# Optimization experiments

Hardware: AMD Instinct MI355X
Metric: run time of the kernel (lower is better)

## Reference

```python
import jax, jax.numpy as jnp
import numpy as np

B, S, D, H = 2, 2048, 2048, 16
HD = D // H  # 128, head_dim (even, as asserted)
MAX_POS = 2048


def setup_inputs() -> dict:
    key = jax.random.key(0)
    ks = jax.random.split(key, 5)
    x = jax.random.normal(ks[0], (B, S, D), jnp.float32)
    Wq = jax.random.normal(ks[1], (D, D), jnp.float32) * 0.02
    Wk = jax.random.normal(ks[2], (D, D), jnp.float32) * 0.02
    Wv = jax.random.normal(ks[3], (D, D), jnp.float32) * 0.02
    Wo = jax.random.normal(ks[4], (D, D), jnp.float32) * 0.02
    # standard RoPE tables: [MAX_POS, HD]
    inv_freq = 1.0 / (10000.0 ** (jnp.arange(0, HD, 2, dtype=jnp.float32) / HD))
    angles = jnp.arange(MAX_POS, dtype=jnp.float32)[:, None] * inv_freq  # [P, HD/2]
    emb = jnp.concatenate([angles, angles], axis=-1)  # [P, HD]
    cos_freqs = jnp.cos(emb)
    sin_freqs = jnp.sin(emb)
    position_ids = jnp.broadcast_to(jnp.arange(S, dtype=jnp.int32), (B, S))
    return {"x": x, "cos_freqs": cos_freqs, "sin_freqs": sin_freqs,
            "Wq": Wq, "Wk": Wk, "Wv": Wv, "Wo": Wo,
            "position_ids": position_ids}


def _apply_rope(t, cos, sin, position_ids):
    # t: [b, s, h, hd]; cos/sin: [P, hd]; position_ids: [b, s]
    c = cos[position_ids][:, :, None, :]  # [b, s, 1, hd]
    s_ = sin[position_ids][:, :, None, :]
    t1, t2 = jnp.split(t, 2, axis=-1)
    rot = jnp.concatenate([-t2, t1], axis=-1)  # rotate-half
    return t * c + rot * s_


def reference(x, cos_freqs, sin_freqs, Wq, Wk, Wv, Wo, position_ids):
    b, s, d = x.shape
    q = (x @ Wq).reshape(b, s, H, HD)
    k = (x @ Wk).reshape(b, s, H, HD)  # n_kv_heads == n_heads
    v = (x @ Wv).reshape(b, s, H, HD)
    q = _apply_rope(q, cos_freqs, sin_freqs, position_ids)
    k = _apply_rope(k, cos_freqs, sin_freqs, position_ids)
    # [b, h, s, hd]
    q_t = jnp.swapaxes(q, 1, 2)
    k_t = jnp.swapaxes(k, 1, 2)
    v_t = jnp.swapaxes(v, 1, 2)
    scale = 1.0 / jnp.sqrt(jnp.float32(HD))
    scores = jnp.einsum('bhsd,bhtd->bhst', q_t, k_t) * scale  # O(s^2) matrix
    causal = jnp.tril(jnp.ones((s, s), dtype=bool))
    scores = jnp.where(causal[None, None, :, :], scores, -1e9)
    weights = jax.nn.softmax(scores, axis=-1)
    out = jnp.einsum('bhst,bhtd->bhsd', weights, v_t)
    out = jnp.swapaxes(out, 1, 2).reshape(b, s, d)
    out = out @ Wo
    return (out, k, v)  # kv_cache is post-RoPE, pre-transpose as in original
```

## Files before the change

kernel.cpp:

```cpp
#include <hip/hip_runtime.h>
#include <hip/hip_bf16.h>
#include <math.h>

#define B_ 2
#define S_ 2048
#define D_ 2048
#define H_ 16
#define HD_ 128
#define M_ (B_*S_)
#define BSD ((size_t)B_*S_*D_)

typedef short bf16x8 __attribute__((ext_vector_type(8)));
typedef float floatx4 __attribute__((ext_vector_type(4)));
typedef __hip_bfloat16 bf16;

union cv8 { bf16 h[8]; uint4 u; bf16x8 v; };

__device__ inline cv8 cvt8(const float4 a, const float4 b) {
    cv8 c;
    c.h[0] = __float2bfloat16(a.x); c.h[1] = __float2bfloat16(a.y);
    c.h[2] = __float2bfloat16(a.z); c.h[3] = __float2bfloat16(a.w);
    c.h[4] = __float2bfloat16(b.x); c.h[5] = __float2bfloat16(b.y);
    c.h[6] = __float2bfloat16(b.z); c.h[7] = __float2bfloat16(b.w);
    return c;
}

__device__ __forceinline__ void gld16(const void* g, void* l) {
    __builtin_amdgcn_global_load_lds(
        (const __attribute__((address_space(1))) unsigned int*)g,
        (__attribute__((address_space(3))) unsigned int*)l,
        16, 0, 0);
}

__global__ __launch_bounds__(256) void transpose_w(
    const float* __restrict__ W, bf16* __restrict__ Wt, int N, int K)
{
    __shared__ float T[32][33];
    const int k0 = blockIdx.x * 32, n0 = blockIdx.y * 32;
    const int r = threadIdx.x >> 3, c4 = (threadIdx.x & 7) * 4;
    float4 v = *(const float4*)&W[(size_t)(k0 + r) * N + n0 + c4];
    T[r][c4+0] = v.x; T[r][c4+1] = v.y; T[r][c4+2] = v.z; T[r][c4+3] = v.w;
    __syncthreads();
    union { bf16 h[4]; uint2 u; } o;
    #pragma unroll
    for (int i = 0; i < 4; ++i) o.h[i] = __float2bfloat16(T[c4 + i][r]);
    *(uint2*)&Wt[(size_t)(n0 + r) * K + k0 + c4] = o.u;
}

__global__ __launch_bounds__(256) void transpose_w_s(
    const float* __restrict__ W, bf16* __restrict__ Wt, int N, int K)
{
    __shared__ float T[32][33];
    const int k0 = blockIdx.x * 32, n0 = blockIdx.y * 32;
    const int r = threadIdx.x >> 3, c4 = (threadIdx.x & 7) * 4;
    float4 v = *(const float4*)&W[(size_t)(k0 + r) * N + n0 + c4];
    T[r][c4+0] = v.x; T[r][c4+1] = v.y; T[r][c4+2] = v.z; T[r][c4+3] = v.w;
    __syncthreads();
    union { bf16 h[4]; uint2 u; } o;
    #pragma unroll
    for (int i = 0; i < 4; ++i) o.h[i] = __float2bfloat16(T[c4 + i][r]);
    const int n = n0 + r;
    size_t bo = (size_t)n * (size_t)K * 2 + ((unsigned)((k0 + c4) * 2) ^ ((n & 3) << 4));
    *(uint2*)((char*)Wt + bo) = o.u;
}

__global__ __launch_bounds__(256) void pack_bf16(
    const float* __restrict__ src, bf16* __restrict__ dst)
{
    const size_t i = ((size_t)blockIdx.x * 256 + threadIdx.x) * 8;
    cv8 c = cvt8(*(const float4*)(src + i), *(const float4*)(src + i + 4));
    size_t bo = i * 2;
    bo ^= (size_t)(((bo >> 12) & 3) << 4);
    *(uint4*)((char*)dst + bo) = c.u;
}

__global__ __launch_bounds__(256) void rope_pack_k(
    float* __restrict__ k, bf16* __restrict__ kbb,
    const float* __restrict__ cf, const float* __restrict__ sf,
    const int* __restrict__ pos)
{
    const int idx = blockIdx.x * 256 + threadIdx.x;
    const int dg = idx & 7;
    const int h  = (idx >> 3) & (H_-1);
    const int bs = idx >> 7;
    const int s  = bs & (S_-1);
    const int b  = bs >> 11;
    const int p  = pos[bs];
    const size_t base = (size_t)bs * D_ + h*HD_ + dg*8;
    float lo[8], hi[8], c1[8], s1[8], c2[8], s2[8];
    *(float4*)&lo[0] = *(const float4*)&k[base];
    *(float4*)&lo[4] = *(const float4*)&k[base + 4];
    *(float4*)&hi[0] = *(const float4*)&k[base + 64];
    *(float4*)&hi[4] = *(const float4*)&k[base + 68];
    const float* cp = cf + (size_t)p*HD_ + dg*8;
    const float* sp = sf + (size_t)p*HD_ + dg*8;
    *(float4*)&c1[0] = *(const float4*)cp;        *(float4*)&c1[4] = *(const float4*)(cp + 4);
    *(float4*)&s1[0] = *(const float4*)sp;        *(float4*)&s1[4] = *(const float4*)(sp + 4);
    *(float4*)&c2[0] = *(const float4*)(cp + 64); *(float4*)&c2[4] = *(const float4*)(cp + 68);
    *(float4*)&s2[0] = *(const float4*)(sp + 64); *(float4*)&s2[4] = *(const float4*)(sp + 68);
    float nl[8], nh[8];
    #pragma unroll
    for (int j = 0; j < 8; ++j) {
        nl[j] = lo[j]*c1[j] - hi[j]*s1[j];
        nh[j] = hi[j]*c2[j] + lo[j]*s2[j];
    }
    *(float4*)&k[base]      = *(float4*)&nl[0];
    *(float4*)&k[base + 4]  = *(float4*)&nl[4];
    *(float4*)&k[base + 64] = *(float4*)&nh[0];
    *(float4*)&k[base + 68] = *(float4*)&nh[4];
    cv8 clo, chi;
    #pragma unroll
    for (int j = 0; j < 8; ++j) {
        clo.h[j] = __float2bfloat16(nl[j]);
        chi.h[j] = __float2bfloat16(nh[j]);
    }
    const size_t rowb = ((size_t)(b*H_ + h)*S_ + s) * (size_t)(HD_*2);
    *(uint4*)((char*)kbb + rowb + ((dg*16)       ^ ((s & 7) << 4))) = clo.u;
    *(uint4*)((char*)kbb + rowb + (((dg+8)*16)   ^ ((s & 7) << 4))) = chi.u;
}

__global__ __launch_bounds__(256) void pack_vt(
    const float* __restrict__ src, bf16* __restrict__ dst)
{
    __shared__ float T[32][33];
    const int s0 = blockIdx.x * 32;
    const int d0 = blockIdx.y * 32;
    const int bh = blockIdx.z;
    const int b = bh >> 4, h = bh & (H_-1);
    const int r = threadIdx.x >> 3, c4 = (threadIdx.x & 7) * 4;
    float4 v = *(const float4*)&src[((size_t)(b*S_ + s0 + r)*H_ + h)*HD_ + d0 + c4];
    T[r][c4+0] = v.x; T[r][c4+1] = v.y; T[r][c4+2] = v.z; T[r][c4+3] = v.w;
    __syncthreads();
    union { bf16 h4[4]; uint2 u; } o;
    #pragma unroll
    for (int i = 0; i < 4; ++i) o.h4[i] = __float2bfloat16(T[c4 + i][r]);
    const int hd = d0 + r;
    size_t rowb = ((size_t)bh*HD_ + hd) * (size_t)(S_*2);
    size_t colb = (size_t)(s0 + c4) * 2;
    colb = (colb & ~(size_t)127) | (((unsigned)colb & 127u) ^ (unsigned)((hd & 7) << 4));
    *(uint2*)((char*)dst + rowb + colb) = o.u;
}

__global__ __launch_bounds__(256, 3) void gemm_bb2(
    const bf16* __restrict__ A, const bf16* __restrict__ Wt,
    float* __restrict__ C, int M, int N, int K)
{
    __shared__ __align__(16) bf16 As[128][32];
    __shared__ __align__(16) bf16 Bs[128][32];
    const int nwg = (int)(gridDim.x * gridDim.y);
    int id = (int)(blockIdx.y * gridDim.x + blockIdx.x);
    if ((nwg & 7) == 0) id = (id & 7) * (nwg >> 3) + (id >> 3);
    const int m0 = (id % (int)gridDim.x) * 128;
    const int n0 = (id / (int)gridDim.x) * 128;
    const int tid = threadIdx.x, lane = tid & 63, w = tid >> 6;
    const int quad = lane >> 4, l16 = lane & 15;
    const int wrow = (w >> 1) * 64, wcol = (w & 1) * 64;
    const size_t K2 = (size_t)K * 2;

    floatx4 acc[4][4] = {};

    const char* Ab = (const char*)A;
    const char* Bb = (const char*)Wt;
    char* AsB = (char*)&As[0][0];
    char* BsB = (char*)&Bs[0][0];
    const int srow = lane >> 2;
    const int scol = (lane & 3) * 16;

    for (int kt = 0; kt < K; kt += 32) {
        #pragma unroll
        for (int j = 0; j < 2; ++j) {
            const int row = w*32 + j*16 + srow;
            gld16(Ab + (size_t)(m0 + row)*K2 + (size_t)(kt*2) + scol,
                  AsB + w*2048 + j*1024);
            gld16(Bb + (size_t)(n0 + row)*K2 + (size_t)(kt*2) + scol,
                  BsB + w*2048 + j*1024);
        }
        __syncthreads();

        bf16x8 af[4], bfr[4];
        #pragma unroll
        for (int t = 0; t < 4; ++t) {
            const int ra = wrow + t*16 + l16;
            af[t]  = *(const bf16x8*)(AsB + ra*64 + ((quad*16) ^ ((ra & 3) << 4)));
            const int rb = wcol + t*16 + l16;
            bfr[t] = *(const bf16x8*)(BsB + rb*64 + ((quad*16) ^ ((rb & 3) << 4)));
        }
        #pragma unroll
        for (int mt = 0; mt < 4; ++mt)
            #pragma unroll
            for (int nt = 0; nt < 4; ++nt)
                acc[mt][nt] = __builtin_amdgcn_mfma_f32_16x16x32_bf16(
                    af[mt], bfr[nt], acc[mt][nt], 0, 0, 0);
        __syncthreads();
    }

    #pragma unroll
    for (int mt = 0; mt < 4; ++mt)
        #pragma unroll
        for (int nt = 0; nt < 4; ++nt)
            #pragma unroll
            for (int r = 0; r < 4; ++r)
                C[(size_t)(m0 + wrow + mt*16 + quad*4 + r) * N
                  + n0 + wcol + nt*16 + l16] = acc[mt][nt][r];
}

__global__ __launch_bounds__(256) void gemm_xw(
    const float* __restrict__ A, const bf16* __restrict__ Wt,
    float* __restrict__ C, int M, int N, int K)
{
    __shared__ __align__(16) bf16 As[128][40];
    __shared__ __align__(16) bf16 Bs[128][40];
    const int m0 = blockIdx.x * 128, n0 = blockIdx.y * 128;
    const int tid = threadIdx.x, lane = tid & 63, w = tid >> 6;
    const int quad = lane >> 4, l16 = lane & 15;
    const int wrow = (w >> 1) * 64, wcol = (w & 1) * 64;
    floatx4 acc[4][4] = {};
    const int arow = tid >> 2;
    const int acol = (tid & 3) * 8;
    for (int kt = 0; kt < K; kt += 32) {
        #pragma unroll
        for (int p = 0; p < 2; ++p) {
            const int r = p*64 + arow;
            const float* ap = &A[(size_t)(m0 + r) * K + kt + acol];
            cv8 ca = cvt8(*(const float4*)ap, *(const float4*)(ap + 4));
            *(uint4*)&As[r][acol] = ca.u;
            const bf16* bp = &Wt[(size_t)(n0 + r) * K + kt + acol];
            *(uint4*)&Bs[r][acol] = *(const uint4*)bp;
        }
        __syncthreads();
        bf16x8 af[4], bfr[4];
        #pragma unroll
        for (int t = 0; t < 4; ++t) {
            af[t]  = *(const bf16x8*)&As[wrow + t*16 + l16][quad*8];
            bfr[t] = *(const bf16x8*)&Bs[wcol + t*16 + l16][quad*8];
        }
        #pragma unroll
        for (int mt = 0; mt < 4; ++mt)
            #pragma unroll
            for (int nt = 0; nt < 4; ++nt)
                acc[mt][nt] = __builtin_amdgcn_mfma_f32_16x16x32_bf16(
                    af[mt], bfr[nt], acc[mt][nt], 0, 0, 0);
        __syncthreads();
    }
    #pragma unroll
    for (int mt = 0; mt < 4; ++mt)
        #pragma unroll
        for (int nt = 0; nt < 4; ++nt)
            #pragma unroll
            for (int r = 0; r < 4; ++r)
                C[(size_t)(m0 + wrow + mt*16 + quad*4 + r) * N
                  + n0 + wcol + nt*16 + l16] = acc[mt][nt][r];
}

__global__ __launch_bounds__(256) void gemm_f32(
    const float* __restrict__ A, const float* __restrict__ W,
    float* __restrict__ C, int M, int N, int K)
{
    __shared__ __align__(16) bf16 As[64][40];
    __shared__ __align__(16) bf16 Bs[64][40];
    const int m0 = blockIdx.x * 64, n0 = blockIdx.y * 64;
    const int tid = threadIdx.x, lane = tid & 63, w = tid >> 6;
    const int quad = lane >> 4, l16 = lane & 15;
    const int wrow = (w >> 1) * 32, wcol = (w & 1) * 32;
    floatx4 acc[2][2] = {};
    const int ar = tid >> 2, ac = (tid & 3) * 8;
    const int br = tid >> 3, bc = (tid & 7) * 8;
    for (int kt = 0; kt < K; kt += 32) {
        {
            const float* ap = &A[(size_t)(m0 + ar) * K + kt + ac];
            cv8 c = cvt8(*(const float4*)ap, *(const float4*)(ap + 4));
            *(uint4*)&As[ar][ac] = c.u;
        }
        {
            const float* wp = &W[(size_t)(kt + br) * N + n0 + bc];
            cv8 c = cvt8(*(const float4*)wp, *(const float4*)(wp + 4));
            #pragma unroll
            for (int i = 0; i < 8; ++i) Bs[bc + i][br] = c.h[i];
        }
        __syncthreads();
        bf16x8 af[2], bfr[2];
        #pragma unroll
        for (int t = 0; t < 2; ++t) {
            af[t]  = *(const bf16x8*)&As[wrow + t*16 + l16][quad*8];
            bfr[t] = *(const bf16x8*)&Bs[wcol + t*16 + l16][quad*8];
        }
        #pragma unroll
        for (int mt = 0; mt < 2; ++mt)
            #pragma unroll
            for (int nt = 0; nt < 2; ++nt)
                acc[mt][nt] = __builtin_amdgcn_mfma_f32_16x16x32_bf16(
                    af[mt], bfr[nt], acc[mt][nt], 0, 0, 0);
        __syncthreads();
    }
    #pragma unroll
    for (int mt = 0; mt < 2; ++mt)
        #pragma unroll
        for (int nt = 0; nt < 2; ++nt)
            #pragma unroll
            for (int r = 0; r < 4; ++r)
                C[(size_t)(m0 + wrow + mt*16 + quad*4 + r) * N
                  + n0 + wcol + nt*16 + l16] = acc[mt][nt][r];
}

__global__ __launch_bounds__(256) void rope_kernel(
    float* __restrict__ q, float* __restrict__ k,
    const float* __restrict__ cf, const float* __restrict__ sf,
    const int* __restrict__ pos)
{
    const int PAIRS = B_*S_*H_*(HD_/2);
    int idx = blockIdx.x * 256 + threadIdx.x;
    float* t = q;
    if (idx >= PAIRS) { t = k; idx -= PAIRS; }
    const int d  = idx & 63;
    const int h  = (idx >> 6) & (H_-1);
    const int bs = idx >> 10;
    const int p  = pos[bs];
    const float c1 = cf[p*HD_ + d],      s1 = sf[p*HD_ + d];
    const float c2 = cf[p*HD_ + d + 64], s2 = sf[p*HD_ + d + 64];
    const size_t base = (size_t)bs * D_ + h*HD_ + d;
    const float t1 = t[base], t2 = t[base + 64];
    t[base]      = t1*c1 - t2*s1;
    t[base + 64] = t2*c2 + t1*s2;
}

__global__ __launch_bounds__(256, 2) void flash_attn_v5(
    const float* __restrict__ qg, const bf16* __restrict__ kb,
    const bf16* __restrict__ vb, bf16* __restrict__ ob,
    const float* __restrict__ cf, const float* __restrict__ sf,
    const int* __restrict__ pos)
{
    __shared__ __align__(16) bf16 Ks[2][64][128];
    __shared__ __align__(16) bf16 Vt[2][128][64];
    __shared__ __align__(16) bf16 Ps[4][16][72];

    const int qi = (int)gridDim.x - 1 - (int)blockIdx.x;
    const int q0 = qi * 64;
    const int bh = blockIdx.y;
    const int b = bh >> 4, h = bh & (H_-1);
    const int tid = threadIdx.x, lane = tid & 63, w = tid >> 6;
    const int quad = lane >> 4, l16 = lane & 15;

    const char* kbase = (const char*)(kb + (size_t)bh * S_ * HD_);
    const char* vbase = (const char*)(vb + (size_t)bh * HD_ * S_);
    char* ksd = (char*)&Ks[0][0][0];
    char* vtd = (char*)&Vt[0][0][0];

    const int klofs = w*4096;
    const int vrow0 = w*32 + (lane >> 3);
    const int vcb   = (lane & 7) * 16;

    #pragma unroll
    for (int j = 0; j < 4; ++j)
        gld16(kbase + klofs + j*1024 + lane*16, ksd + klofs + j*1024);
    #pragma unroll
    for (int j = 0; j < 4; ++j)
        gld16(vbase + (size_t)(vrow0 + j*8)*(S_*2) + vcb, vtd + w*4096 + j*1024);

    const int qrow = q0 + w*16 + l16;
    const float* qptr = qg + ((size_t)(b*S_ + qrow))*D_ + h*HD_;
    float rq[4][8];
    #pragma unroll
    for (int c = 0; c < 4; ++c) {
        const float* qp = qptr + c*32 + quad*8;
        *(float4*)&rq[c][0] = *(const float4*)qp;
        *(float4*)&rq[c][4] = *(const float4*)(qp + 4);
    }
    const int p = pos[b*S_ + qrow];
    bf16x8 qf[4];
    #pragma unroll
    for (int c = 0; c < 4; ++c) {
        const float* cp = cf + (size_t)p*HD_ + c*32 + quad*8;
        const float* sp = sf + (size_t)p*HD_ + c*32 + quad*8;
        float cc[8], ss[8];
        *(float4*)&cc[0] = *(const float4*)cp; *(float4*)&cc[4] = *(const float4*)(cp+4);
        *(float4*)&ss[0] = *(const float4*)sp; *(float4*)&ss[4] = *(const float4*)(sp+4);
        cv8 cv;
        #pragma unroll
        for (int j = 0; j < 8; ++j) {
            const float o = (c < 2) ? rq[c][j]*cc[j] - rq[c^2][j]*ss[j]
                                    : rq[c][j]*cc[j] + rq[c^2][j]*ss[j];
            cv.h[j] = __float2bfloat16(o);
        }
        qf[c] = cv.v;
    }

    floatx4 acc_o[8] = {};
    float m_run[4], l_run[4];
    #pragma unroll
    for (int r = 0; r < 4; ++r) { m_run[r] = -30000.0f; l_run[r] = 0.f; }

    const float SCL2 = 0.08838834764831845f * 1.4426950408889634f;

    __syncthreads();

    for (int kt = 0; kt <= qi; ++kt) {
        const int cur = kt & 1;
        const char* ksb = ksd + cur*16384;
        const char* vtb = vtd + cur*16384;

        bf16x8 kf[4][4];
        #pragma unroll
        for (int c = 0; c < 4; ++c)
            #pragma unroll
            for (int kc = 0; kc < 4; ++kc)
                kf[c][kc] = *(const bf16x8*)(ksb + (c*16 + l16)*256
                              + ((kc*64 + quad*16) ^ ((l16 & 7) << 4)));

        if (kt < qi) {
            const char* ksrc = kbase + (size_t)(kt+1)*16384;
            char* kdst = ksd + (cur^1)*16384;
            #pragma unroll
            for (int j = 0; j < 4; ++j)
                gld16(ksrc + klofs + j*1024 + lane*16, kdst + klofs + j*1024);
            const char* vsrc = vbase + (size_t)(kt+1)*128;
            char* vdst = vtd + (cur^1)*16384;
            #pragma unroll
            for (int j = 0; j < 4; ++j)
                gld16(vsrc + (size_t)(vrow0 + j*8)*(S_*2) + vcb,
                      vdst + w*4096 + j*1024);
        }

        floatx4 sc[4] = {};
        __builtin_amdgcn_s_setprio(1);
        #pragma unroll
        for (int c = 0; c < 4; ++c)
            #pragma unroll
            for (int kc = 0; kc < 4; ++kc)
                sc[c] = __builtin_amdgcn_mfma_f32_16x16x32_bf16(qf[kc], kf[c][kc], sc[c], 0, 0, 0);
        __builtin_amdgcn_s_setprio(0);

        const int k0 = kt * 64;
        float pv[4][4], mt_[4];
        #pragma unroll
        for (int r = 0; r < 4; ++r) mt_[r] = -30000.0f;
        #pragma unroll
        for (int c = 0; c < 4; ++c) {
            const int kcol = k0 + c*16 + l16;
            #pragma unroll
            for (int r = 0; r < 4; ++r) {
                const int qr = q0 + w*16 + quad*4 + r;
                float s = sc[c][r] * SCL2;
                if (kcol > qr) s = -30000.0f;
                pv[c][r] = s;
                mt_[r] = fmaxf(mt_[r], s);
            }
        }
        #pragma unroll
        for (int off = 1; off < 16; off <<= 1)
            #pragma unroll
            for (int r = 0; r < 4; ++r)
                mt_[r] = fmaxf(mt_[r], __shfl_xor(mt_[r], off, 64));
        float alpha[4];
        #pragma unroll
        for (int r = 0; r < 4; ++r) {
            float mn = fmaxf(m_run[r], mt_[r]);
            alpha[r] = exp2f(m_run[r] - mn);
            m_run[r] = mn;
        }
        #pragma unroll
        for (int c = 0; c < 4; ++c)
            #pragma unroll
            for (int r = 0; r < 4; ++r)
                pv[c][r] = exp2f(pv[c][r] - m_run[r]);
        #pragma unroll
        for (int r = 0; r < 4; ++r) {
            float s = pv[0][r] + pv[1][r] + pv[2][r] + pv[3][r];
            #pragma unroll
            for (int off = 1; off < 16; off <<= 1)
                s += __shfl_xor(s, off, 64);
            l_run[r] = l_run[r] * alpha[r] + s;
        }
        #pragma unroll
        for (int c = 0; c < 4; ++c)
            #pragma unroll
            for (int r = 0; r < 4; ++r)
                Ps[w][quad*4 + r][c*16 + l16] = __float2bfloat16(pv[c][r]);

        #pragma unroll
        for (int n = 0; n < 8; ++n)
            #pragma unroll
            for (int r = 0; r < 4; ++r)
                acc_o[n][r] *= alpha[r];
        bf16x8 pf[2];
        #pragma unroll
        for (int kc2 = 0; kc2 < 2; ++kc2)
            pf[kc2] = *(const bf16x8*)&Ps[w][l16][kc2*32 + quad*8];
        bf16x8 vf[8][2];
        #pragma unroll
        for (int n = 0; n < 8; ++n)
            #pragma unroll
            for (int kc2 = 0; kc2 < 2; ++kc2)
                vf[n][kc2] = *(const bf16x8*)(vtb + (n*16 + l16)*128
                               + ((kc2*64 + quad*16) ^ ((l16 & 7) << 4)));
        __builtin_amdgcn_s_setprio(1);
        #pragma unroll
        for (int n = 0; n < 8; ++n)
            #pragma unroll
            for (int kc2 = 0; kc2 < 2; ++kc2)
                acc_o[n] = __builtin_amdgcn_mfma_f32_16x16x32_bf16(pf[kc2], vf[n][kc2], acc_o[n], 0, 0, 0);
        __builtin_amdgcn_s_setprio(0);

        __syncthreads();
    }

    float inv[4];
    #pragma unroll
    for (int r = 0; r < 4; ++r) inv[r] = 1.0f / l_run[r];
    #pragma unroll
    for (int n = 0; n < 8; ++n)
        #pragma unroll
        for (int r = 0; r < 4; ++r) {
            const int qr = q0 + w*16 + quad*4 + r;
            size_t bo = ((((size_t)(b*S_ + qr))*D_ + h*HD_ + n*16 + l16) * 2)
                        ^ (size_t)(r << 4);
            *(bf16*)((char*)ob + bo) = __float2bfloat16(acc_o[n][r] * inv[r]);
        }
}

__global__ __launch_bounds__(256) void flash_attn(
    const float* qg, const float* __restrict__ kg,
    const float* __restrict__ vg, float* og)
{
    __shared__ __align__(16) bf16 Ks[64][136];
    __shared__ __align__(16) bf16 Vt[128][72];
    __shared__ __align__(16) bf16 Ps[4][16][72];

    const int qi = (int)gridDim.x - 1 - (int)blockIdx.x;
    const int q0 = qi * 64;
    const int bh = blockIdx.y;
    const int b = bh >> 4, h = bh & (H_-1);
    const int tid = threadIdx.x, lane = tid & 63, w = tid >> 6;
    const int quad = lane >> 4, l16 = lane & 15;

    const int qrow = q0 + w*16 + l16;
    const float* qptr = qg + ((size_t)(b*S_ + qrow)*H_ + h)*HD_;
    bf16x8 qf[4];
    #pragma unroll
    for (int c = 0; c < 4; ++c) {
        const float* qp = qptr + c*32 + quad*8;
        cv8 cv = cvt8(*(const float4*)qp, *(const float4*)(qp + 4));
        qf[c] = cv.v;
    }

    floatx4 acc_o[8] = {};
    float m_run[4], l_run[4];
    #pragma unroll
    for (int r = 0; r < 4; ++r) { m_run[r] = -30000.0f; l_run[r] = 0.f; }

    const int ksr = tid >> 2, kscg = (tid & 3) * 32;
    const int vk2 = (tid & 31) * 2, vf8 = (tid >> 5) * 8;

    for (int kt = 0; kt <= qi; ++kt) {
        const int k0 = kt * 64;
        {
            const float* kp = kg + ((size_t)(b*S_ + k0 + ksr)*H_ + h)*HD_ + kscg;
            #pragma unroll
            for (int j = 0; j < 4; ++j) {
                cv8 c = cvt8(*(const float4*)(kp + j*8), *(const float4*)(kp + j*8 + 4));
                *(uint4*)&Ks[ksr][kscg + j*8] = c.u;
            }
        }
        {
            #pragma unroll
            for (int pq = 0; pq < 2; ++pq) {
                const int f = vf8 + pq*64;
                const float* v0p = vg + ((size_t)(b*S_ + k0 + vk2)*H_ + h)*HD_ + f;
                const float* v1p = v0p + D_;
                cv8 c0 = cvt8(*(const float4*)v0p, *(const float4*)(v0p + 4));
                cv8 c1 = cvt8(*(const float4*)v1p, *(const float4*)(v1p + 4));
                #pragma unroll
                for (int i = 0; i < 8; ++i) {
                    union { bf16 h2[2]; unsigned u; } pk;
                    pk.h2[0] = c0.h[i]; pk.h2[1] = c1.h[i];
                    *(unsigned*)&Vt[f + i][vk2] = pk.u;
                }
            }
        }
        __syncthreads();

        floatx4 sc[4] = {};
        #pragma unroll
        for (int c = 0; c < 4; ++c)
            #pragma unroll
            for (int kc = 0; kc < 4; ++kc) {
                bf16x8 kf = *(const bf16x8*)&Ks[c*16 + l16][kc*32 + quad*8];
                sc[c] = __builtin_amdgcn_mfma_f32_16x16x32_bf16(qf[kc], kf, sc[c], 0, 0, 0);
            }

        float pv[4][4], mt_[4];
        #pragma unroll
        for (int r = 0; r < 4; ++r) mt_[r] = -30000.0f;
        #pragma unroll
        for (int c = 0; c < 4; ++c) {
            const int kcol = k0 + c*16 + l16;
            #pragma unroll
            for (int r = 0; r < 4; ++r) {
                const int qr = q0 + w*16 + quad*4 + r;
                float s = sc[c][r] * 0.08838834764831845f;
                if (kcol > qr) s = -30000.0f;
                pv[c][r] = s;
                mt_[r] = fmaxf(mt_[r], s);
            }
        }
        #pragma unroll
        for (int off = 1; off < 16; off <<= 1)
            #pragma unroll
            for (int r = 0; r < 4; ++r)
                mt_[r] = fmaxf(mt_[r], __shfl_xor(mt_[r], off, 64));
        float alpha[4];
        #pragma unroll
        for (int r = 0; r < 4; ++r) {
            float mn = fmaxf(m_run[r], mt_[r]);
            alpha[r] = __expf(m_run[r] - mn);
            m_run[r] = mn;
        }
        #pragma unroll
        for (int c = 0; c < 4; ++c)
            #pragma unroll
            for (int r = 0; r < 4; ++r)
                pv[c][r] = __expf(pv[c][r] - m_run[r]);
        #pragma unroll
        for (int r = 0; r < 4; ++r) {
            float s = pv[0][r] + pv[1][r] + pv[2][r] + pv[3][r];
            #pragma unroll
            for (int off = 1; off < 16; off <<= 1)
                s += __shfl_xor(s, off, 64);
            l_run[r] = l_run[r] * alpha[r] + s;
        }
        #pragma unroll
        for (int c = 0; c < 4; ++c)
            #pragma unroll
            for (int r = 0; r < 4; ++r)
                Ps[w][quad*4 + r][c*16 + l16] = __float2bfloat16(pv[c][r]);
        __syncthreads();

        #pragma unroll
        for (int n = 0; n < 8; ++n)
            #pragma unroll
            for (int r = 0; r < 4; ++r)
                acc_o[n][r] *= alpha[r];
        bf16x8 pf[2];
        #pragma unroll
        for (int kc2 = 0; kc2 < 2; ++kc2)
            pf[kc2] = *(const bf16x8*)&Ps[w][l16][kc2*32 + quad*8];
        #pragma unroll
        for (int n = 0; n < 8; ++n)
            #pragma unroll
            for (int kc2 = 0; kc2 < 2; ++kc2) {
                bf16x8 vf = *(const bf16x8*)&Vt[n*16 + l16][kc2*32 + quad*8];
                acc_o[n] = __builtin_amdgcn_mfma_f32_16x16x32_bf16(pf[kc2], vf, acc_o[n], 0, 0, 0);
            }
        __syncthreads();
    }

    #pragma unroll
    for (int n = 0; n < 8; ++n)
        #pragma unroll
        for (int r = 0; r < 4; ++r) {
            const int qr = q0 + w*16 + quad*4 + r;
            og[((size_t)(b*S_ + qr))*D_ + h*HD_ + n*16 + l16] = acc_o[n][r] / l_run[r];
        }
}

extern "C" void kernel_launch(void* const* d_in, const int* in_sizes, int n_in,
                              void* d_out, int out_size, void* d_ws, size_t ws_size,
                              hipStream_t stream) {
    const float* x  = (const float*)d_in[0];
    const float* cf = (const float*)d_in[1];
    const float* sf = (const float*)d_in[2];
    const float* Wq = (const float*)d_in[3];
    const float* Wk = (const float*)d_in[4];
    const float* Wv = (const float*)d_in[5];
    const float* Wo = (const float*)d_in[6];
    const int*  pos = (const int*)d_in[7];

    float* out  = (float*)d_out;
    float* kout = out + BSD;
    float* vout = out + 2*BSD;

    const size_t WT_BYTES = (size_t)D_ * D_ * sizeof(bf16);
    const size_t TB_BYTES = BSD * sizeof(bf16);
    const size_t NEED_V5  = WT_BYTES + 4 * TB_BYTES;
    const bool big = ws_size >= WT_BYTES + (size_t)128 * D_ * sizeof(float);

    if (ws_size >= NEED_V5) {
        bf16* wt  = (bf16*)d_ws;
        bf16* xb  = wt + (size_t)D_ * D_;
        bf16* kbb = xb + BSD;
        bf16* vbb = kbb + BSD;
        bf16* obb = vbb + BSD;

        dim3 tg(D_/32, D_/32), gg(M_/128, D_/128);
        pack_bf16<<<(int)(BSD/8/256), 256, 0, stream>>>(x, xb);
        transpose_w_s<<<tg, 256, 0, stream>>>(Wq, wt, D_, D_);
        gemm_bb2<<<gg, 256, 0, stream>>>(xb, wt, out,  M_, D_, D_);
        transpose_w_s<<<tg, 256, 0, stream>>>(Wk, wt, D_, D_);
        gemm_bb2<<<gg, 256, 0, stream>>>(xb, wt, kout, M_, D_, D_);
        transpose_w_s<<<tg, 256, 0, stream>>>(Wv, wt, D_, D_);
        gemm_bb2<<<gg, 256, 0, stream>>>(xb, wt, vout, M_, D_, D_);
        rope_pack_k<<<(B_*S_*H_*8)/256, 256, 0, stream>>>(kout, kbb, cf, sf, pos);
        pack_vt<<<dim3(S_/32, HD_/32, B_*H_), 256, 0, stream>>>(vout, vbb);
        flash_attn_v5<<<dim3(S_/64, B_*H_), 256, 0, stream>>>(out, kbb, vbb, obb,
                                                              cf, sf, pos);
        transpose_w_s<<<tg, 256, 0, stream>>>(Wo, wt, D_, D_);
        gemm_bb2<<<gg, 256, 0, stream>>>(obb, wt, out, M_, D_, D_);
    } else if (big) {
        bf16*  wt  = (bf16*)d_ws;
        float* cws = (float*)((char*)d_ws + WT_BYTES);
        const size_t crem = ws_size - WT_BYTES;
        dim3 tg(D_/32, D_/32), gg(M_/128, D_/128);
        transpose_w<<<tg, 256, 0, stream>>>(Wq, wt, D_, D_);
        gemm_xw<<<gg, 256, 0, stream>>>(x, wt, out,  M_, D_, D_);
        transpose_w<<<tg, 256, 0, stream>>>(Wk, wt, D_, D_);
        gemm_xw<<<gg, 256, 0, stream>>>(x, wt, kout, M_, D_, D_);
        transpose_w<<<tg, 256, 0, stream>>>(Wv, wt, D_, D_);
        gemm_xw<<<gg, 256, 0, stream>>>(x, wt, vout, M_, D_, D_);
        rope_kernel<<<(2*B_*S_*H_*(HD_/2))/256, 256, 0, stream>>>(out, kout, cf, sf, pos);
        flash_attn<<<dim3(S_/64, B_*H_), 256, 0, stream>>>(out, kout, vout, out);
        transpose_w<<<tg, 256, 0, stream>>>(Wo, wt, D_, D_);
        int R = 128;
        while (R < M_ && (size_t)(2*R) * D_ * sizeof(float) <= crem) R *= 2;
        for (int m0 = 0; m0 < M_; m0 += R) {
            gemm_xw<<<dim3(R/128, D_/128), 256, 0, stream>>>(out + (size_t)m0*D_, wt, cws, R, D_, D_);
            hipMemcpyAsync(out + (size_t)m0*D_, cws, (size_t)R*D_*sizeof(float),
                           hipMemcpyDeviceToDevice, stream);
        }
    } else {
        float* wsb = (float*)d_ws;
        dim3 gg(M_/64, D_/64);
        gemm_f32<<<gg, 256, 0, stream>>>(x, Wq, out,  M_, D_, D_);
        gemm_f32<<<gg, 256, 0, stream>>>(x, Wk, kout, M_, D_, D_);
        gemm_f32<<<gg, 256, 0, stream>>>(x, Wv, vout, M_, D_, D_);
        rope_kernel<<<(2*B_*S_*H_*(HD_/2))/256, 256, 0, stream>>>(out, kout, cf, sf, pos);
        flash_attn<<<dim3(S_/64, B_*H_), 256, 0, stream>>>(out, kout, vout, out);
        int R = 64;
        while (R < M_ && (size_t)(2*R) * D_ * sizeof(float) <= ws_size) R *= 2;
        if ((size_t)R * D_ * sizeof(float) > ws_size) R = 64;
        for (int m0 = 0; m0 < M_; m0 += R) {
            gemm_f32<<<dim3(R/64, D_/64), 256, 0, stream>>>(out + (size_t)m0*D_, Wo, wsb, R, D_, D_);
            hipMemcpyAsync(out + (size_t)m0*D_, wsb, (size_t)R*D_*sizeof(float),
                           hipMemcpyDeviceToDevice, stream);
        }
    }
}
```

Measured before the change: 592.6 us.

## Transpose QK^T MFMA so softmax is per-lane and drop P LDS staging

The flash attention kernel swaps the MFMA operands so each lane owns one query row of the score tile. Row max and sum then need only two cross-quad shuffles instead of sixteen-lane reductions, and P is redistributed into the PV operand layout through shuffles rather than an LDS buffer. The V tile becomes single-buffered and is loaded within the current iteration. K and V fragments are read from LDS just before each MFMA, and launch bounds rise to three blocks per CU. The aim is lower register and LDS pressure and less reduction overhead, at the cost of losing V prefetch overlap, an extra barrier per tile, and many shuffles to build P fragments.

```diff
diff --git a/kernel.cpp b/kernel.cpp
--- a/kernel.cpp
+++ b/kernel.cpp
@@ -1,6 +1,5 @@
 #include <hip/hip_runtime.h>
 #include <hip/hip_bf16.h>
-#include <math.h>
 
 #define B_ 2
 #define S_ 2048
@@ -323,15 +322,14 @@
     t[base + 64] = t2*c2 + t1*s2;
 }
 
-__global__ __launch_bounds__(256, 2) void flash_attn_v5(
+__global__ __launch_bounds__(256, 3) void flash_attn_v6(
     const float* __restrict__ qg, const bf16* __restrict__ kb,
     const bf16* __restrict__ vb, bf16* __restrict__ ob,
     const float* __restrict__ cf, const float* __restrict__ sf,
     const int* __restrict__ pos)
 {
     __shared__ __align__(16) bf16 Ks[2][64][128];
-    __shared__ __align__(16) bf16 Vt[2][128][64];
-    __shared__ __align__(16) bf16 Ps[4][16][72];
+    __shared__ __align__(16) bf16 Vt[128][64];
 
     const int qi = (int)gridDim.x - 1 - (int)blockIdx.x;
     const int q0 = qi * 64;
@@ -343,7 +341,7 @@
     const char* kbase = (const char*)(kb + (size_t)bh * S_ * HD_);
     const char* vbase = (const char*)(vb + (size_t)bh * HD_ * S_);
     char* ksd = (char*)&Ks[0][0][0];
-    char* vtd = (char*)&Vt[0][0][0];
+    char* vtd = (char*)&Vt[0][0];
 
     const int klofs = w*4096;
     const int vrow0 = w*32 + (lane >> 3);
@@ -352,9 +350,6 @@
     #pragma unroll
     for (int j = 0; j < 4; ++j)
         gld16(kbase + klofs + j*1024 + lane*16, ksd + klofs + j*1024);
-    #pragma unroll
-    for (int j = 0; j < 4; ++j)
-        gld16(vbase + (size_t)(vrow0 + j*8)*(S_*2) + vcb, vtd + w*4096 + j*1024);
 
     const int qrow = q0 + w*16 + l16;
     const float* qptr = qg + ((size_t)(b*S_ + qrow))*D_ + h*HD_;
@@ -385,26 +380,15 @@
     }
 
     floatx4 acc_o[8] = {};
-    float m_run[4], l_run[4];
-    #pragma unroll
-    for (int r = 0; r < 4; ++r) { m_run[r] = -30000.0f; l_run[r] = 0.f; }
-
-    const float SCL2 = 0.08838834764831845f * 1.4426950408889634f;
+    float m_run = -30000.0f, l_run = 0.0f;
+    const int qr_sm = q0 + w*16 + l16;
+    const float SCL = 0.08838834764831845f;
 
     __syncthreads();
 
     for (int kt = 0; kt <= qi; ++kt) {
         const int cur = kt & 1;
         const char* ksb = ksd + cur*16384;
-        const char* vtb = vtd + cur*16384;
-
-        bf16x8 kf[4][4];
-        #pragma unroll
-        for (int c = 0; c < 4; ++c)
-            #pragma unroll
-            for (int kc = 0; kc < 4; ++kc)
-                kf[c][kc] = *(const bf16x8*)(ksb + (c*16 + l16)*256
-                              + ((kc*64 + quad*16) ^ ((l16 & 7) << 4)));
 
         if (kt < qi) {
             const char* ksrc = kbase + (size_t)(kt+1)*16384;
@@ -412,12 +396,13 @@
             #pragma unroll
             for (int j = 0; j < 4; ++j)
                 gld16(ksrc + klofs + j*1024 + lane*16, kdst + klofs + j*1024);
-            const char* vsrc = vbase + (size_t)(kt+1)*128;
-            char* vdst = vtd + (cur^1)*16384;
+        }
+        {
+            const char* vsrc = vbase + (size_t)kt*128;
             #pragma unroll
             for (int j = 0; j < 4; ++j)
                 gld16(vsrc + (size_t)(vrow0 + j*8)*(S_*2) + vcb,
-                      vdst + w*4096 + j*1024);
+                      vtd + w*4096 + j*1024);
         }
 
         floatx4 sc[4] = {};
@@ -425,87 +410,93 @@
         #pragma unroll
         for (int c = 0; c < 4; ++c)
             #pragma unroll
-            for (int kc = 0; kc < 4; ++kc)
-                sc[c] = __builtin_amdgcn_mfma_f32_16x16x32_bf16(qf[kc], kf[c][kc], sc[c], 0, 0, 0);
+            for (int kc = 0; kc < 4; ++kc) {
+                bf16x8 kf = *(const bf16x8*)(ksb + (c*16 + l16)*256
+                              + ((kc*64 + quad*16) ^ ((l16 & 7) << 4)));
+                sc[c] = __builtin_amdgcn_mfma_f32_16x16x32_bf16(kf, qf[kc], sc[c], 0, 0, 0);
+            }
         __builtin_amdgcn_s_setprio(0);
 
         const int k0 = kt * 64;
-        float pv[4][4], mt_[4];
-        #pragma unroll
-        for (int r = 0; r < 4; ++r) mt_[r] = -30000.0f;
+        float pv[4][4], mt = -30000.0f;
+        #pragma unroll
+        for (int c = 0; c < 4; ++c)
+            #pragma unroll
+            for (int r = 0; r < 4; ++r) {
+                const int kcol = k0 + c*16 + quad*4 + r;
+                float s = sc[c][r] * SCL;
+                if (kcol > qr_sm) s = -30000.0f;
+                pv[c][r] = s;
+                mt = fmaxf(mt, s);
+            }
+        mt = fmaxf(mt, __shfl_xor(mt, 16, 64));
+        mt = fmaxf(mt, __shfl_xor(mt, 32, 64));
+        const float mn = fmaxf(m_run, mt);
+        const float alpha = __expf(m_run - mn);
+        m_run = mn;
+        float sum = 0.0f;
+        #pragma unroll
+        for (int c = 0; c < 4; ++c)
+            #pragma unroll
+            for (int r = 0; r < 4; ++r) {
+                pv[c][r] = __expf(pv[c][r] - mn);
+                sum += pv[c][r];
+            }
+        sum += __shfl_xor(sum, 16, 64);
+        sum += __shfl_xor(sum, 32, 64);
+        l_run = l_run * alpha + sum;
+
+        float at[4];
+        #pragma unroll
+        for (int r = 0; r < 4; ++r) at[r] = __shfl(alpha, quad*4 + r, 64);
+        #pragma unroll
+        for (int n = 0; n < 8; ++n)
+            #pragma unroll
+            for (int r = 0; r < 4; ++r)
+                acc_o[n][r] *= at[r];
+
+        unsigned pk[4][2];
         #pragma unroll
         for (int c = 0; c < 4; ++c) {
-            const int kcol = k0 + c*16 + l16;
-            #pragma unroll
-            for (int r = 0; r < 4; ++r) {
-                const int qr = q0 + w*16 + quad*4 + r;
-                float s = sc[c][r] * SCL2;
-                if (kcol > qr) s = -30000.0f;
-                pv[c][r] = s;
-                mt_[r] = fmaxf(mt_[r], s);
-            }
-        }
-        #pragma unroll
-        for (int off = 1; off < 16; off <<= 1)
-            #pragma unroll
-            for (int r = 0; r < 4; ++r)
-                mt_[r] = fmaxf(mt_[r], __shfl_xor(mt_[r], off, 64));
-        float alpha[4];
-        #pragma unroll
-        for (int r = 0; r < 4; ++r) {
-            float mn = fmaxf(m_run[r], mt_[r]);
-            alpha[r] = exp2f(m_run[r] - mn);
-            m_run[r] = mn;
-        }
-        #pragma unroll
-        for (int c = 0; c < 4; ++c)
-            #pragma unroll
-            for (int r = 0; r < 4; ++r)
-                pv[c][r] = exp2f(pv[c][r] - m_run[r]);
-        #pragma unroll
-        for (int r = 0; r < 4; ++r) {
-            float s = pv[0][r] + pv[1][r] + pv[2][r] + pv[3][r];
-            #pragma unroll
-            for (int off = 1; off < 16; off <<= 1)
-                s += __shfl_xor(s, off, 64);
-            l_run[r] = l_run[r] * alpha[r] + s;
-        }
-        #pragma unroll
-        for (int c = 0; c < 4; ++c)
-            #pragma unroll
-            for (int r = 0; r < 4; ++r)
-                Ps[w][quad*4 + r][c*16 + l16] = __float2bfloat16(pv[c][r]);
-
+            union { bf16 h2[2]; unsigned u; } a0, a1;
+            a0.h2[0] = __float2bfloat16(pv[c][0]); a0.h2[1] = __float2bfloat16(pv[c][1]);
+            a1.h2[0] = __float2bfloat16(pv[c][2]); a1.h2[1] = __float2bfloat16(pv[c][3]);
+            pk[c][0] = a0.u; pk[c][1] = a1.u;
+        }
+        bf16x8 pf[2];
+        #pragma unroll
+        for (int kc2 = 0; kc2 < 2; ++kc2) {
+            union { unsigned u[4]; bf16x8 v; } wv;
+            #pragma unroll
+            for (int u_ = 0; u_ < 4; ++u_) {
+                const int sl = ((quad & 1)*2 + (u_ >> 1))*16 + l16;
+                const unsigned w0 = __shfl(pk[kc2*2 + 0][u_ & 1], sl, 64);
+                const unsigned w1 = __shfl(pk[kc2*2 + 1][u_ & 1], sl, 64);
+                wv.u[u_] = (quad >> 1) ? w1 : w0;
+            }
+            pf[kc2] = wv.v;
+        }
+
+        __syncthreads();
+
+        __builtin_amdgcn_s_setprio(1);
         #pragma unroll
         for (int n = 0; n < 8; ++n)
             #pragma unroll
-            for (int r = 0; r < 4; ++r)
-                acc_o[n][r] *= alpha[r];
-        bf16x8 pf[2];
-        #pragma unroll
-        for (int kc2 = 0; kc2 < 2; ++kc2)
-            pf[kc2] = *(const bf16x8*)&Ps[w][l16][kc2*32 + quad*8];
-        bf16x8 vf[8][2];
-        #pragma unroll
-        for (int n = 0; n < 8; ++n)
-            #pragma unroll
-            for (int kc2 = 0; kc2 < 2; ++kc2)
-                vf[n][kc2] = *(const bf16x8*)(vtb + (n*16 + l16)*128
+            for (int kc2 = 0; kc2 < 2; ++kc2) {
+                bf16x8 vf = *(const bf16x8*)(vtd + (n*16 + l16)*128
                                + ((kc2*64 + quad*16) ^ ((l16 & 7) << 4)));
-        __builtin_amdgcn_s_setprio(1);
-        #pragma unroll
-        for (int n = 0; n < 8; ++n)
-            #pragma unroll
-            for (int kc2 = 0; kc2 < 2; ++kc2)
-                acc_o[n] = __builtin_amdgcn_mfma_f32_16x16x32_bf16(pf[kc2], vf[n][kc2], acc_o[n], 0, 0, 0);
+                acc_o[n] = __builtin_amdgcn_mfma_f32_16x16x32_bf16(pf[kc2], vf, acc_o[n], 0, 0, 0);
+            }
         __builtin_amdgcn_s_setprio(0);
 
         __syncthreads();
     }
 
-    float inv[4];
-    #pragma unroll
-    for (int r = 0; r < 4; ++r) inv[r] = 1.0f / l_run[r];
+    const float linv = 1.0f / l_run;
+    float lt[4];
+    #pragma unroll
+    for (int r = 0; r < 4; ++r) lt[r] = __shfl(linv, quad*4 + r, 64);
     #pragma unroll
     for (int n = 0; n < 8; ++n)
         #pragma unroll
@@ -513,7 +504,7 @@
             const int qr = q0 + w*16 + quad*4 + r;
             size_t bo = ((((size_t)(b*S_ + qr))*D_ + h*HD_ + n*16 + l16) * 2)
                         ^ (size_t)(r << 4);
-            *(bf16*)((char*)ob + bo) = __float2bfloat16(acc_o[n][r] * inv[r]);
+            *(bf16*)((char*)ob + bo) = __float2bfloat16(acc_o[n][r] * lt[r]);
         }
 }
 
@@ -680,10 +671,10 @@
 
     const size_t WT_BYTES = (size_t)D_ * D_ * sizeof(bf16);
     const size_t TB_BYTES = BSD * sizeof(bf16);
-    const size_t NEED_V5  = WT_BYTES + 4 * TB_BYTES;
+    const size_t NEED_V6  = WT_BYTES + 4 * TB_BYTES;
     const bool big = ws_size >= WT_BYTES + (size_t)128 * D_ * sizeof(float);
 
-    if (ws_size >= NEED_V5) {
+    if (ws_size >= NEED_V6) {
         bf16* wt  = (bf16*)d_ws;
         bf16* xb  = wt + (size_t)D_ * D_;
         bf16* kbb = xb + BSD;
@@ -700,7 +691,7 @@
         gemm_bb2<<<gg, 256, 0, stream>>>(xb, wt, vout, M_, D_, D_);
         rope_pack_k<<<(B_*S_*H_*8)/256, 256, 0, stream>>>(kout, kbb, cf, sf, pos);
         pack_vt<<<dim3(S_/32, HD_/32, B_*H_), 256, 0, stream>>>(vout, vbb);
-        flash_attn_v5<<<dim3(S_/64, B_*H_), 256, 0, stream>>>(out, kbb, vbb, obb,
+        flash_attn_v6<<<dim3(S_/64, B_*H_), 256, 0, stream>>>(out, kbb, vbb, obb,
                                                               cf, sf, pos);
         transpose_w_s<<<tg, 256, 0, stream>>>(Wo, wt, D_, D_);
         gemm_bb2<<<gg, 256, 0, stream>>>(obb, wt, out, M_, D_, D_);
```

New measurement: 557.1 us. 6.0% less time.
